# Kernel optimization log

Hardware: AMD Instinct MI355X
Metric: run time of the kernel (lower is better)

## Reference

```python
import jax, jax.numpy as jnp
import numpy as np

B, S, D = 4, 4096, 1024
WINDOW = 129
HALF = WINDOW // 2  # 64
NEG = -1e9


def setup_inputs() -> dict:
    key = jax.random.key(0)
    ks = jax.random.split(key, 7)
    sc = 1.0 / np.sqrt(D).astype(np.float32)
    x = jax.random.normal(ks[0], (B, S, D), dtype=jnp.float32)
    Wq = jax.random.normal(ks[1], (D, D), dtype=jnp.float32) * sc
    Wk = jax.random.normal(ks[2], (D, D), dtype=jnp.float32) * sc
    Wv = jax.random.normal(ks[3], (D, D), dtype=jnp.float32) * sc
    bq = jax.random.normal(ks[4], (D,), dtype=jnp.float32) * 0.01
    bk = jax.random.normal(ks[5], (D,), dtype=jnp.float32) * 0.01
    bv = jax.random.normal(ks[6], (D,), dtype=jnp.float32) * 0.01
    return {"x": x, "Wq": Wq, "bq": bq, "Wk": Wk, "bk": bk, "Wv": Wv, "bv": bv}


def reference(x, Wq, bq, Wk, bk, Wv, bv):
    # Linear projections (torch Linear: x @ W.T + b)
    Q = x @ Wq.T + bq  # [B,S,D]
    K = x @ Wk.T + bk
    V = x @ Wv.T + bv
    # Banded additive mask: 0 inside |i-j|<=HALF, -1e9 outside
    idx = jnp.arange(S)
    mask = jnp.where(jnp.abs(idx[:, None] - idx[None, :]) <= HALF, 0.0, NEG).astype(x.dtype)
    scale = jnp.sqrt(jnp.asarray(D, dtype=x.dtype))
    scores = jnp.einsum('bqd,bkd->bqk', Q, K) / scale + mask  # [B,S,S]
    attn_weights = jax.nn.softmax(scores, axis=-1)
    output = jnp.einsum('bqk,bkd->bqd', attn_weights, V)  # [B,S,D]
    return (output, attn_weights)
```

## Files before the change

### kernel.cpp

```cpp
#include <hip/hip_runtime.h>
#include <stdint.h>

#define B_ 4
#define S_ 4096
#define D_ 1024
#define HALF_ 64
#define NPACK 3072

typedef __attribute__((ext_vector_type(4))) float f32x4;
typedef __attribute__((ext_vector_type(8))) short short8;
typedef __attribute__((ext_vector_type(4))) short short4v;
typedef __attribute__((ext_vector_type(4))) float float4v;

__device__ __forceinline__ short f2bf(float f) {
  union { float f; uint32_t u; } x;
  x.f = f;
  uint32_t u = x.u;
  uint32_t r = (u + 0x7FFFu + ((u >> 16) & 1u)) >> 16;
  return (short)(r & 0xFFFFu);
}

__device__ __forceinline__ void gload_lds16(const void* g, void* l) {
  __builtin_amdgcn_global_load_lds(
      (const __attribute__((address_space(1))) void*)g,
      (__attribute__((address_space(3))) void*)l, 16, 0, 0);
}

__global__ __launch_bounds__(256) void cast_f32_to_bf16(
    const float* __restrict__ in, short* __restrict__ out, int n4) {
  int stride = gridDim.x * blockDim.x;
  for (int i = blockIdx.x * blockDim.x + threadIdx.x; i < n4; i += stride) {
    float4v v = *(const float4v*)(in + (size_t)i * 4);
    short4v o;
    o.x = f2bf(v.x);
    o.y = f2bf(v.y);
    o.z = f2bf(v.z);
    o.w = f2bf(v.w);
    *(short4v*)(out + (size_t)i * 4) = o;
  }
}

__global__ __launch_bounds__(256) void pack_bias(
    const float* __restrict__ bq, const float* __restrict__ bk,
    const float* __restrict__ bv, float* __restrict__ out) {
  int i = blockIdx.x * blockDim.x + threadIdx.x;
  const float* src = (i < 1024) ? bq : ((i < 2048) ? bk : bv);
  out[i] = src[i & 1023];
}

__global__ __launch_bounds__(256) void gemm_bias_bf16(
    const short* __restrict__ A, const short* __restrict__ Bw,
    const float* __restrict__ bias, short* __restrict__ C,
    int M, int N, int K) {
  __shared__ __align__(16) short Asm[128 * 64];
  __shared__ __align__(16) short Bsm[128 * 64];
  const int tid = threadIdx.x;
  const int l = tid & 63;
  const int w = tid >> 6;
  const int nt = N >> 7;
  const int m0 = (blockIdx.x / nt) << 7;
  const int n0 = (blockIdx.x % nt) << 7;
  const int wr = w >> 1, wc = w & 1;

  f32x4 acc[4][4];
#pragma unroll
  for (int i = 0; i < 4; ++i)
#pragma unroll
    for (int j = 0; j < 4; ++j) acc[i][j] = (f32x4){0.f, 0.f, 0.f, 0.f};

  int srow[4], scol[4], slds[4];
#pragma unroll
  for (int r = 0; r < 4; ++r) {
    int q = r * 4096 + w * 1024 + l * 16;
    srow[r] = q >> 7;
    scol[r] = (q & 127) >> 1;
    slds[r] = (r * 4096 + w * 1024) >> 1;
  }

  const int kiters = K >> 6;
  for (int kt = 0; kt < kiters; ++kt) {
    const int kb = kt << 6;
#pragma unroll
    for (int r = 0; r < 4; ++r) {
      gload_lds16(A + (size_t)(m0 + srow[r]) * K + kb + scol[r], &Asm[slds[r]]);
      gload_lds16(Bw + (size_t)(n0 + srow[r]) * K + kb + scol[r], &Bsm[slds[r]]);
    }
    __syncthreads();
#pragma unroll
    for (int ks = 0; ks < 2; ++ks) {
      short8 af[4], bf[4];
#pragma unroll
      for (int mi = 0; mi < 4; ++mi)
        af[mi] = *(const short8*)&Asm[((wr << 6) + (mi << 4) + (l & 15)) * 64 +
                                      (ks << 5) + ((l >> 4) << 3)];
#pragma unroll
      for (int ni = 0; ni < 4; ++ni)
        bf[ni] = *(const short8*)&Bsm[((wc << 6) + (ni << 4) + (l & 15)) * 64 +
                                      (ks << 5) + ((l >> 4) << 3)];
#pragma unroll
      for (int mi = 0; mi < 4; ++mi)
#pragma unroll
        for (int ni = 0; ni < 4; ++ni)
          acc[mi][ni] = __builtin_amdgcn_mfma_f32_16x16x32_bf16(
              af[mi], bf[ni], acc[mi][ni], 0, 0, 0);
    }
    __syncthreads();
  }

#pragma unroll
  for (int ni = 0; ni < 4; ++ni) {
    const int col = n0 + (wc << 6) + (ni << 4) + (l & 15);
    const float bv = bias[col];
#pragma unroll
    for (int mi = 0; mi < 4; ++mi) {
      const int row = m0 + (wr << 6) + (mi << 4) + ((l >> 4) << 2);
#pragma unroll
      for (int r = 0; r < 4; ++r)
        C[(size_t)(row + r) * N + col] = f2bf(acc[mi][ni][r] + bv);
    }
  }
}

__global__ __launch_bounds__(256) void transpose_v_packed(
    const short* __restrict__ QKV, short* __restrict__ Vt) {
  __shared__ __align__(16) short t[64][72];
  const int i0 = blockIdx.x << 6;
  const int d0 = blockIdx.y << 6;
  const int b = blockIdx.z;
  const int tid = threadIdx.x;
  const int lr = tid >> 3;
  const int lc = (tid & 7) << 3;
#pragma unroll
  for (int rr = 0; rr < 2; ++rr) {
    int row = (rr << 5) + lr;
    short8 v = *(const short8*)&QKV[((size_t)b * S_ + i0 + row) * NPACK + 2048 +
                                    d0 + lc];
    *(short8*)&t[row][lc] = v;
  }
  __syncthreads();
#pragma unroll
  for (int rr = 0; rr < 2; ++rr) {
    int drow = (rr << 5) + lr;
    short8 v;
#pragma unroll
    for (int q = 0; q < 8; ++q) v[q] = t[lc + q][drow];
    *(short8*)&Vt[((size_t)b * D_ + d0 + drow) * S_ + i0 + lc] = v;
  }
}

__global__ __launch_bounds__(256, 1) void swa_fused(
    const short* __restrict__ QKV, const short* __restrict__ Vtb,
    float* __restrict__ outO, float* __restrict__ outW) {
  __shared__ __align__(16) short P_lds[4][16][200];
  const int tid = threadIdx.x;
  const int l = tid & 63;
  const int w = tid >> 6;
  const int b = blockIdx.y;
  const int i0 = blockIdx.x << 6;
  const int iw = i0 + (w << 4);
  const int j0 = i0 - 64;
  const int lq = l & 15;
  const int lg = l >> 4;

  f32x4 acc[12];
#pragma unroll
  for (int jc = 0; jc < 12; ++jc) acc[jc] = (f32x4){0.f, 0.f, 0.f, 0.f};

  const short* qptr = QKV + ((size_t)b * S_ + iw + lq) * NPACK + (lg << 3);
  const short* kptr[12];
#pragma unroll
  for (int jc = 0; jc < 12; ++jc) {
    int j = j0 + (jc << 4) + lq;
    int jcl = j < 0 ? 0 : (j > S_ - 1 ? S_ - 1 : j);
    kptr[jc] = QKV + ((size_t)b * S_ + jcl) * NPACK + 1024 + (lg << 3);
  }
#pragma unroll 2
  for (int d0 = 0; d0 < D_; d0 += 32) {
    short8 qa = *(const short8*)(qptr + d0);
#pragma unroll
    for (int jc = 0; jc < 12; ++jc) {
      short8 kv = *(const short8*)(kptr[jc] + d0);
      acc[jc] = __builtin_amdgcn_mfma_f32_16x16x32_bf16(qa, kv, acc[jc], 0, 0, 0);
    }
  }

  const float scale = 0.03125f;
#pragma unroll
  for (int r = 0; r < 4; ++r) {
    const int i = iw + (lg << 2) + r;
    float sv[12];
    float m = -3.0e38f;
#pragma unroll
    for (int jc = 0; jc < 12; ++jc) {
      int j = j0 + (jc << 4) + lq;
      bool valid = (j >= i - HALF_) && (j <= i + HALF_) && (j >= 0) && (j < S_);
      float s = acc[jc][r] * scale;
      sv[jc] = valid ? s : -3.0e38f;
      m = fmaxf(m, sv[jc]);
    }
#pragma unroll
    for (int mk = 1; mk <= 8; mk <<= 1) m = fmaxf(m, __shfl_xor(m, mk, 64));
    float p[12];
    float sum = 0.f;
#pragma unroll
    for (int jc = 0; jc < 12; ++jc) {
      p[jc] = (sv[jc] > -1.0e38f) ? __expf(sv[jc] - m) : 0.f;
      sum += p[jc];
    }
#pragma unroll
    for (int mk = 1; mk <= 8; mk <<= 1) sum += __shfl_xor(sum, mk, 64);
    const float inv = 1.0f / sum;
    float* wrow = outW + ((size_t)b * S_ + i) * S_;
#pragma unroll
    for (int jc = 0; jc < 12; ++jc) {
      int j = j0 + (jc << 4) + lq;
      float pw = p[jc] * inv;
      if (j >= 0 && j < S_) wrow[j] = pw;
      P_lds[w][(lg << 2) + r][(jc << 4) + lq] = f2bf(pw);
    }
  }

  {
    const int L0 = j0 < 0 ? 0 : j0;
    const int R0 = (j0 + 192 > S_) ? S_ : (j0 + 192);
    const float4v z4 = {0.f, 0.f, 0.f, 0.f};
#pragma unroll 4
    for (int rr = 0; rr < 16; ++rr) {
      float* rowp = outW + ((size_t)b * S_ + iw + rr) * S_;
      for (int c = l << 2; c < L0; c += 256) *(float4v*)(rowp + c) = z4;
      for (int c = R0 + (l << 2); c < S_; c += 256) *(float4v*)(rowp + c) = z4;
    }
  }

  __syncthreads();

  short8 pa[6];
#pragma unroll
  for (int ks = 0; ks < 6; ++ks)
    pa[ks] = *(const short8*)&P_lds[w][lq][(ks << 5) + (lg << 3)];

  const short* vbase = Vtb + ((size_t)b * D_ + lq) * S_;
  int joff[6];
#pragma unroll
  for (int ks = 0; ks < 6; ++ks) {
    int j = j0 + (ks << 5) + (lg << 3);
    joff[ks] = j < 0 ? 0 : (j > S_ - 8 ? S_ - 8 : j);
  }
  float* obase = outO + ((size_t)b * S_ + iw + (lg << 2)) * D_ + lq;
#pragma unroll 2
  for (int dc = 0; dc < 64; ++dc) {
    f32x4 o = (f32x4){0.f, 0.f, 0.f, 0.f};
    const short* vd = vbase + ((size_t)(dc << 4)) * S_;
#pragma unroll
    for (int ks = 0; ks < 6; ++ks) {
      short8 vv = *(const short8*)(vd + joff[ks]);
      o = __builtin_amdgcn_mfma_f32_16x16x32_bf16(pa[ks], vv, o, 0, 0, 0);
    }
#pragma unroll
    for (int r = 0; r < 4; ++r) obase[(size_t)r * D_ + (dc << 4)] = o[r];
  }
}

extern "C" void kernel_launch(void* const* d_in, const int* in_sizes, int n_in,
                              void* d_out, int out_size, void* d_ws, size_t ws_size,
                              hipStream_t stream) {
  (void)in_sizes; (void)n_in; (void)out_size; (void)ws_size;
  const float* x  = (const float*)d_in[0];
  const float* Wq = (const float*)d_in[1];
  const float* bq = (const float*)d_in[2];
  const float* Wk = (const float*)d_in[3];
  const float* bk = (const float*)d_in[4];
  const float* Wv = (const float*)d_in[5];
  const float* bv = (const float*)d_in[6];

  const size_t NX = (size_t)B_ * S_ * D_;
  const size_t NW = (size_t)D_ * D_;
  const int M = B_ * S_;

  char* ws = (char*)d_ws;
  size_t off = 0;
  short* xb    = (short*)(ws + off); off += NX * 2;
  short* Wqkvb = (short*)(ws + off); off += 3 * NW * 2;
  float* bias3 = (float*)(ws + off); off += NPACK * sizeof(float);
  short* QKVp  = (short*)(ws + off); off += (size_t)M * NPACK * 2;
  short* Vtb   = (short*)(ws + off); off += NX * 2;

  float* outO = (float*)d_out;
  float* outW = outO + NX;

  cast_f32_to_bf16<<<4096, 256, 0, stream>>>(x, xb, (int)(NX / 4));
  cast_f32_to_bf16<<<1024, 256, 0, stream>>>(Wq, Wqkvb, (int)(NW / 4));
  cast_f32_to_bf16<<<1024, 256, 0, stream>>>(Wk, Wqkvb + NW, (int)(NW / 4));
  cast_f32_to_bf16<<<1024, 256, 0, stream>>>(Wv, Wqkvb + 2 * NW, (int)(NW / 4));
  pack_bias<<<12, 256, 0, stream>>>(bq, bk, bv, bias3);

  dim3 ggrid((M / 128) * (NPACK / 128));
  gemm_bias_bf16<<<ggrid, 256, 0, stream>>>(xb, Wqkvb, bias3, QKVp, M, NPACK, D_);

  transpose_v_packed<<<dim3(S_ / 64, D_ / 64, B_), 256, 0, stream>>>(QKVp, Vtb);

  swa_fused<<<dim3(S_ / 64, B_), 256, 0, stream>>>(QKVp, Vtb, outO, outW);
}
```

Measured before the change: 669.1 us.

## Restructure QKV GEMM with LDS-resident weight slab, memset mask zeros, merge casts

After: 725.7 us. 8.5% more time.

```diff
diff --git a/kernel.cpp b/kernel.cpp
--- a/kernel.cpp
+++ b/kernel.cpp
@@ -40,6 +40,31 @@
   }
 }
 
+__global__ __launch_bounds__(256) void cast_w3(
+    const float* __restrict__ Wq, const float* __restrict__ Wk,
+    const float* __restrict__ Wv, short* __restrict__ out, int per) {
+  const int total = 3 * per;
+  const int stride = gridDim.x * blockDim.x;
+  for (int i = blockIdx.x * blockDim.x + threadIdx.x; i < total; i += stride) {
+    const float* src;
+    int j = i;
+    if (i < per) {
+      src = Wq;
+    } else if (i < 2 * per) {
+      src = Wk; j = i - per;
+    } else {
+      src = Wv; j = i - 2 * per;
+    }
+    float4v v = *(const float4v*)(src + (size_t)j * 4);
+    short4v o;
+    o.x = f2bf(v.x);
+    o.y = f2bf(v.y);
+    o.z = f2bf(v.z);
+    o.w = f2bf(v.w);
+    *(short4v*)(out + (size_t)i * 4) = o;
+  }
+}
+
 __global__ __launch_bounds__(256) void pack_bias(
     const float* __restrict__ bq, const float* __restrict__ bk,
     const float* __restrict__ bv, float* __restrict__ out) {
@@ -48,19 +73,31 @@
   out[i] = src[i & 1023];
 }
 
-__global__ __launch_bounds__(256) void gemm_bias_bf16(
+__global__ __launch_bounds__(512, 2) void gemm_wres(
     const short* __restrict__ A, const short* __restrict__ Bw,
-    const float* __restrict__ bias, short* __restrict__ C,
-    int M, int N, int K) {
-  __shared__ __align__(16) short Asm[128 * 64];
-  __shared__ __align__(16) short Bsm[128 * 64];
+    const float* __restrict__ bias, short* __restrict__ C) {
+  __shared__ __align__(16) char Bl[64 * 2048];
   const int tid = threadIdx.x;
   const int l = tid & 63;
   const int w = tid >> 6;
-  const int nt = N >> 7;
-  const int m0 = (blockIdx.x / nt) << 7;
-  const int n0 = (blockIdx.x % nt) << 7;
-  const int wr = w >> 1, wc = w & 1;
+  const int lq = l & 15, lg = l >> 4;
+
+  const int bid = blockIdx.x;
+  const int swz = ((bid & 7) * 192) + (bid >> 3);
+  const int m0 = (swz / 48) * 512;
+  const int n0 = (swz % 48) * 64;
+
+#pragma unroll
+  for (int c = 0; c < 16; ++c) {
+    const int base = c * 8192 + w * 1024;
+    const int n = base >> 11;
+    const int k2 = (base & 2047) + l * 16;
+    const int xo = (n & 7) << 4;
+    const char* src = (const char*)Bw + (((size_t)(n0 + n)) << 11) + (k2 ^ xo);
+    gload_lds16(src, Bl + base);
+  }
+  asm volatile("s_waitcnt vmcnt(0)");
+  __syncthreads();
 
   f32x4 acc[4][4];
 #pragma unroll
@@ -68,35 +105,22 @@
 #pragma unroll
     for (int j = 0; j < 4; ++j) acc[i][j] = (f32x4){0.f, 0.f, 0.f, 0.f};
 
-  int srow[4], scol[4], slds[4];
-#pragma unroll
-  for (int r = 0; r < 4; ++r) {
-    int q = r * 4096 + w * 1024 + l * 16;
-    srow[r] = q >> 7;
-    scol[r] = (q & 127) >> 1;
-    slds[r] = (r * 4096 + w * 1024) >> 1;
-  }
-
-  const int kiters = K >> 6;
-  for (int kt = 0; kt < kiters; ++kt) {
-    const int kb = kt << 6;
-#pragma unroll
-    for (int r = 0; r < 4; ++r) {
-      gload_lds16(A + (size_t)(m0 + srow[r]) * K + kb + scol[r], &Asm[slds[r]]);
-      gload_lds16(Bw + (size_t)(n0 + srow[r]) * K + kb + scol[r], &Bsm[slds[r]]);
-    }
-    __syncthreads();
+  const short* Arow = A + (size_t)(m0 + w * 64) * 1024;
+
+  for (int kc = 0; kc < 16; ++kc) {
 #pragma unroll
     for (int ks = 0; ks < 2; ++ks) {
+      const int ko = kc * 64 + ks * 32 + lg * 8;
       short8 af[4], bf[4];
 #pragma unroll
       for (int mi = 0; mi < 4; ++mi)
-        af[mi] = *(const short8*)&Asm[((wr << 6) + (mi << 4) + (l & 15)) * 64 +
-                                      (ks << 5) + ((l >> 4) << 3)];
-#pragma unroll
-      for (int ni = 0; ni < 4; ++ni)
-        bf[ni] = *(const short8*)&Bsm[((wc << 6) + (ni << 4) + (l & 15)) * 64 +
-                                      (ks << 5) + ((l >> 4) << 3)];
+        af[mi] = *(const short8*)(Arow + (size_t)(mi * 16 + lq) * 1024 + ko);
+#pragma unroll
+      for (int ni = 0; ni < 4; ++ni) {
+        const int nn = ni * 16 + lq;
+        const int kb2 = ko * 2;
+        bf[ni] = *(const short8*)(Bl + nn * 2048 + (kb2 ^ ((nn & 7) << 4)));
+      }
 #pragma unroll
       for (int mi = 0; mi < 4; ++mi)
 #pragma unroll
@@ -104,19 +128,18 @@
           acc[mi][ni] = __builtin_amdgcn_mfma_f32_16x16x32_bf16(
               af[mi], bf[ni], acc[mi][ni], 0, 0, 0);
     }
-    __syncthreads();
   }
 
 #pragma unroll
   for (int ni = 0; ni < 4; ++ni) {
-    const int col = n0 + (wc << 6) + (ni << 4) + (l & 15);
-    const float bv = bias[col];
+    const int col = n0 + ni * 16 + lq;
+    const float bvv = bias[col];
 #pragma unroll
     for (int mi = 0; mi < 4; ++mi) {
-      const int row = m0 + (wr << 6) + (mi << 4) + ((l >> 4) << 2);
+      const int row = m0 + w * 64 + mi * 16 + (lg << 2);
 #pragma unroll
       for (int r = 0; r < 4; ++r)
-        C[(size_t)(row + r) * N + col] = f2bf(acc[mi][ni][r] + bv);
+        C[(size_t)(row + r) * NPACK + col] = f2bf(acc[mi][ni][r] + bvv);
     }
   }
 }
@@ -220,20 +243,6 @@
     }
   }
 
-  {
-    const int L0 = j0 < 0 ? 0 : j0;
-    const int R0 = (j0 + 192 > S_) ? S_ : (j0 + 192);
-    const float4v z4 = {0.f, 0.f, 0.f, 0.f};
-#pragma unroll 4
-    for (int rr = 0; rr < 16; ++rr) {
-      float* rowp = outW + ((size_t)b * S_ + iw + rr) * S_;
-      for (int c = l << 2; c < L0; c += 256) *(float4v*)(rowp + c) = z4;
-      for (int c = R0 + (l << 2); c < S_; c += 256) *(float4v*)(rowp + c) = z4;
-    }
-  }
-
-  __syncthreads();
-
   short8 pa[6];
 #pragma unroll
   for (int ks = 0; ks < 6; ++ks)
@@ -288,14 +297,13 @@
   float* outO = (float*)d_out;
   float* outW = outO + NX;
 
-  cast_f32_to_bf16<<<4096, 256, 0, stream>>>(x, xb, (int)(NX / 4));
-  cast_f32_to_bf16<<<1024, 256, 0, stream>>>(Wq, Wqkvb, (int)(NW / 4));
-  cast_f32_to_bf16<<<1024, 256, 0, stream>>>(Wk, Wqkvb + NW, (int)(NW / 4));
-  cast_f32_to_bf16<<<1024, 256, 0, stream>>>(Wv, Wqkvb + 2 * NW, (int)(NW / 4));
+  hipMemsetAsync(outW, 0, (size_t)B_ * S_ * S_ * sizeof(float), stream);
+
+  cast_f32_to_bf16<<<2048, 256, 0, stream>>>(x, xb, (int)(NX / 4));
+  cast_w3<<<3072, 256, 0, stream>>>(Wq, Wk, Wv, Wqkvb, (int)(NW / 4));
   pack_bias<<<12, 256, 0, stream>>>(bq, bk, bv, bias3);
 
-  dim3 ggrid((M / 128) * (NPACK / 128));
-  gemm_bias_bf16<<<ggrid, 256, 0, stream>>>(xb, Wqkvb, bias3, QKVp, M, NPACK, D_);
+  gemm_wres<<<1536, 512, 0, stream>>>(xb, Wqkvb, bias3, QKVp);
 
   transpose_v_packed<<<dim3(S_ / 64, D_ / 64, B_), 256, 0, stream>>>(QKVp, Vtb);
 
```
